# Kernel optimization log

Measured on AMD Instinct MI355X. Metric: run time of the kernel, lower is better.

The kernel has to match this reference:

```python
import jax, jax.numpy as jnp
import numpy as np

D = 256; HD = 16; G = 16; L = 2; HOP = 2; HK = 4
N = 16384; E = 49152; B = 256
VA = 128; VB = 8
SQRT2PI = float(np.sqrt(2.0 * 3.14159))  # module uses pi=3.14159


def group_norm(x, g=G, eps=1e-5):
    # torch GroupNorm(affine=False) on [N, D, 1]: normalize over each group of D//g channels
    n, d = x.shape
    xg = x.reshape(n, g, d // g)
    m = xg.mean(-1, keepdims=True)
    v = ((xg - m) ** 2).mean(-1, keepdims=True)
    return ((xg - m) * jax.lax.rsqrt(v + eps)).reshape(n, d)


def glin(x, w):
    # grouped 1x1 conv (no bias): x [n, g*din], w [g, dout, din] -> [n, g*dout]
    g, dout, din = w.shape
    return jnp.einsum('ngd,god->ngo', x.reshape(-1, g, din), w).reshape(-1, g * dout)


def multi_embed(idx, tables):
    # OGB-style encoder: sum of per-feature embeddings. idx [M,F], tables [F,V,D]
    out = tables[0][idx[:, 0]]
    for f in range(1, tables.shape[0]):
        out = out + tables[f][idx[:, f]]
    return out


def glb(x, pre_w, pre_b, gate_w, val_w, post_w, post_b):
    # GatedLinearBlock (dropout is identity in eval)
    xx = group_norm(x @ pre_w.T + pre_b)
    xx = jax.nn.relu(glin(xx, gate_w)) * glin(xx, val_w)
    return xx @ post_w.T + post_b


def glb2(xg, xv, gate_w, val_w, post_w, post_b):
    # GatedLinearBlock2: separate gate/value inputs, GroupNorm first
    gg = jax.nn.relu(glin(group_norm(xg), gate_w))
    vv = glin(group_norm(xv), val_w)
    return (gg * vv) @ post_w.T + post_b


def forward_impl(x_feat, edge_index, edge_attr, batch, batch_size,
                 edge_distance, atom_emb, bond2d_emb, gauss_means, gauss_stds,
                 attn_w, attn_b, scale_both,
                 conv_bond_emb, conv_pre_w, conv_gate_w, conv_val_w, conv_post_w, conv_post_b, conv_scale,
                 virt_pre_w, virt_pre_b, virt_gate_w, virt_val_w, virt_post_w, virt_post_b, virt_scale,
                 att_pre_w, att_pre_b, att_q_w, att_k_w, att_v_w, att_post_w, att_post_b, att_scale,
                 main_pre_w, main_pre_b, main_gate_w, main_val_w, main_post_w, main_post_b):
    src, dst = edge_index[0], edge_index[1]
    n = x_feat.shape[0]
    deg = jnp.clip(jax.ops.segment_sum(jnp.ones_like(dst), dst, num_segments=n) - 1, 0, 3)
    # --- edge features, mode='both': fuse 2D bond embedding with 3D gaussian features ---
    h2d = multi_embed(edge_attr, bond2d_emb)                      # [E, D]
    std = jnp.abs(gauss_stds) + 0.01
    diff = (edge_distance[:, None] - gauss_means[None, :]) / std
    h3d = jnp.exp(-0.5 * diff * diff) / (SQRT2PI * std)          # [E, D]
    w = jax.nn.sigmoid(jnp.concatenate([h2d, h3d], axis=-1) @ attn_w + attn_b[0])[:, None]
    h_e = w * h2d + (1.0 - w) * h3d
    h_in = jnp.exp(scale_both)[deg] * jax.ops.segment_sum(h_e, dst, num_segments=n)
    h_in = multi_embed(x_feat, atom_emb) + h_in                   # [N, D]
    h_virt = jnp.zeros((batch_size, D), h_in.dtype)
    h_att = jnp.zeros((batch_size, 2 * D // HD, HD, HD), h_in.dtype)
    for l in range(L):
        # --- ConvMessage: hop*kernel gated message-passing sublayers ---
        x_raw, x_out = h_in, jnp.zeros_like(h_in)
        for k in range(HK):
            if k > 0 and k % HOP == 0:
                x_raw, x_out = h_in + x_out, jnp.zeros_like(h_in)
            bond = multi_embed(edge_attr, conv_bond_emb[l, k])
            xp = x_raw @ conv_pre_w[l, k].T
            msg = glb2(xp[dst] + bond, xp[src] + bond,
                       conv_gate_w[l, k], conv_val_w[l, k], conv_post_w[l, k], conv_post_b[l, k])
            x_raw = jax.ops.segment_sum(msg, dst, num_segments=n)
            x_out = x_out + jnp.exp(conv_scale[l, k])[deg] * x_raw
        h_out = h_in + x_out
        # --- VirtMessage: graph-level virtual node with residual state ---
        h_virt = jax.ops.segment_sum(h_in, batch, num_segments=batch_size) + h_virt
        h_out = h_out + (jnp.exp(virt_scale[l]) * glb(h_virt, virt_pre_w[l], virt_pre_b[l],
                          virt_gate_w[l], virt_val_w[l], virt_post_w[l], virt_post_b[l]))[batch]
        # --- AttMessage: linear attention with per-graph scatter normalization ---
        xv0 = group_norm(h_in @ att_pre_w[l].T + att_pre_b[l])
        xq = jnp.exp(glin(xv0, att_q_w[l]) / np.sqrt(HD)).reshape(n, -1, HD)   # [N,32,16]
        xk = jnp.exp(glin(xv0, att_k_w[l]) / np.sqrt(HD)).reshape(n, -1, HD)
        xv = glin(xv0, att_v_w[l]).reshape(n, -1, HD)
        xkv = jnp.einsum('bnh,bnv->bnhv', xk, xv)                               # [N,32,16,16]
        h_att = jax.ops.segment_sum(xkv, batch, num_segments=batch_size) + h_att
        xk_sum = jax.ops.segment_sum(xk, batch, num_segments=batch_size)[batch]
        xq = xq / jnp.einsum('bnh,bnh->bn', xq, xk_sum)[:, :, None]
        att_out = jnp.einsum('bnh,bnhv->bnv', xq, h_att[batch]).reshape(n, 2 * D)
        h_out = h_out + jnp.exp(att_scale[l]) * (att_out @ att_post_w[l].T + att_post_b[l])
        # --- main gated block ---
        h_in = glb(h_out, main_pre_w[l], main_pre_b[l],
                   main_gate_w[l], main_val_w[l], main_post_w[l], main_post_b[l])
    return h_in


def setup_inputs() -> dict:
    key = jax.random.key(0)
    ks = iter(jax.random.split(key, 80))
    def rn(shape, s=0.05):
        return jax.random.normal(next(ks), shape, dtype=jnp.float32) * s
    inp = {}
    inp['x_feat'] = jax.random.randint(next(ks), (N, 9), 0, VA)
    inp['edge_index'] = jax.random.randint(next(ks), (2, E), 0, N)
    inp['edge_attr'] = jax.random.randint(next(ks), (E, 3), 0, VB)
    inp['batch'] = jnp.sort(jax.random.randint(next(ks), (N,), 0, B))
    inp['batch_size'] = B
    inp['edge_distance'] = jax.random.uniform(next(ks), (E,), dtype=jnp.float32) * 4.0
    inp['atom_emb'] = rn((9, VA, D))
    inp['bond2d_emb'] = rn((3, VB, D))
    inp['gauss_means'] = jax.random.uniform(next(ks), (D,), minval=2.0, maxval=3.0)
    inp['gauss_stds'] = jax.random.uniform(next(ks), (D,), minval=1.0, maxval=1.5)
    inp['attn_w'] = rn((2 * D,))
    inp['attn_b'] = rn((1,))
    inp['scale_both'] = jnp.full((4, D), np.log(0.1), jnp.float32)
    inp['conv_bond_emb'] = rn((L, HK, 3, VB, D))
    inp['conv_pre_w'] = rn((L, HK, D, D))
    inp['conv_gate_w'] = rn((L, HK, G, HD, HD))
    inp['conv_val_w'] = rn((L, HK, G, HD, HD))
    inp['conv_post_w'] = rn((L, HK, D, D))
    inp['conv_post_b'] = rn((L, HK, D))
    inp['conv_scale'] = jnp.full((L, HK, 4, D), np.log(0.1), jnp.float32)
    inp['virt_pre_w'] = rn((L, D, D)); inp['virt_pre_b'] = rn((L, D))
    inp['virt_gate_w'] = rn((L, G, 2 * HD, HD)); inp['virt_val_w'] = rn((L, G, 2 * HD, HD))
    inp['virt_post_w'] = rn((L, D, 2 * D)); inp['virt_post_b'] = rn((L, D))
    inp['virt_scale'] = jnp.full((L, D), np.log(0.01), jnp.float32)
    inp['att_pre_w'] = rn((L, D, D)); inp['att_pre_b'] = rn((L, D))
    inp['att_q_w'] = rn((L, G, 2 * HD, HD)); inp['att_k_w'] = rn((L, G, 2 * HD, HD)); inp['att_v_w'] = rn((L, G, 2 * HD, HD))
    inp['att_post_w'] = rn((L, D, 2 * D)); inp['att_post_b'] = rn((L, D))
    inp['att_scale'] = jnp.full((L, D), np.log(0.01), jnp.float32)
    inp['main_pre_w'] = rn((L, D, D)); inp['main_pre_b'] = rn((L, D))
    inp['main_gate_w'] = rn((L, G, 3 * HD, HD)); inp['main_val_w'] = rn((L, G, 3 * HD, HD))
    inp['main_post_w'] = rn((L, D, 3 * D)); inp['main_post_b'] = rn((L, D))
    return inp


def reference(x_feat, edge_index, edge_attr, batch, batch_size, edge_distance,
              atom_emb, bond2d_emb, gauss_means, gauss_stds, attn_w, attn_b, scale_both,
              conv_bond_emb, conv_pre_w, conv_gate_w, conv_val_w, conv_post_w, conv_post_b, conv_scale,
              virt_pre_w, virt_pre_b, virt_gate_w, virt_val_w, virt_post_w, virt_post_b, virt_scale,
              att_pre_w, att_pre_b, att_q_w, att_k_w, att_v_w, att_post_w, att_post_b, att_scale,
              main_pre_w, main_pre_b, main_gate_w, main_val_w, main_post_w, main_post_b):
    return forward_impl(x_feat, edge_index, edge_attr, batch, batch_size,
                        edge_distance, atom_emb, bond2d_emb, gauss_means, gauss_stds,
                        attn_w, attn_b, scale_both,
                        conv_bond_emb, conv_pre_w, conv_gate_w, conv_val_w, conv_post_w, conv_post_b, conv_scale,
                        virt_pre_w, virt_pre_b, virt_gate_w, virt_val_w, virt_post_w, virt_post_b, virt_scale,
                        att_pre_w, att_pre_b, att_q_w, att_k_w, att_v_w, att_post_w, att_post_b, att_scale,
                        main_pre_w, main_pre_b, main_gate_w, main_val_w, main_post_w, main_post_b)
```

## Files before the change

kernel.cpp:

```cpp
#include <hip/hip_runtime.h>
#include <cstdint>
#include <cstddef>
#include <type_traits>

#define NN 16384
#define EE 49152
#define BB 256

typedef _Float16 f16;
typedef _Float16 half8 __attribute__((ext_vector_type(8)));
typedef _Float16 half4v __attribute__((ext_vector_type(4)));
typedef _Float16 half2v __attribute__((ext_vector_type(2)));
typedef float floatx4 __attribute__((ext_vector_type(4)));

#if defined(__has_builtin)
#if __has_builtin(__builtin_amdgcn_fdot2)
#define HAVE_FDOT2 1
#endif
#endif

static constexpr size_t ND = (size_t)NN * 256;


__global__ __launch_bounds__(256) void count_deg_kernel(const int* __restrict__ dst, int* __restrict__ cnt, int e) {
  int i = blockIdx.x * 256 + threadIdx.x;
  if (i < e) atomicAdd(&cnt[dst[i]], 1);
}
__global__ __launch_bounds__(256) void clip_deg_kernel(const int* __restrict__ cnt, int* __restrict__ deg, int n) {
  int i = blockIdx.x * 256 + threadIdx.x;
  if (i < n) { int v = cnt[i] - 1; deg[i] = v < 0 ? 0 : (v > 3 ? 3 : v); }
}
__global__ __launch_bounds__(256) void goff_kernel(const int* __restrict__ batch, int* __restrict__ goff, int n, int b) {
  int i = blockIdx.x * 256 + threadIdx.x;
  if (i > n) return;
  int cur = (i < n) ? batch[i] : b;
  int prev = (i == 0) ? -1 : batch[i - 1];
  for (int x = prev + 1; x <= cur; x++) goff[x] = i;
}
__global__ __launch_bounds__(256) void scan_off_kernel(const int* __restrict__ cnt, int* __restrict__ off) {
  __shared__ int part[256];
  int tid = threadIdx.x;
  int base = tid * 64;
  int s = 0;
  for (int i = 0; i < 64; i++) s += cnt[base + i];
  part[tid] = s;
  __syncthreads();
  for (int o = 1; o < 256; o <<= 1) {
    int t = (tid >= o) ? part[tid - o] : 0;
    __syncthreads();
    part[tid] += t;
    __syncthreads();
  }
  int run = (tid == 0) ? 0 : part[tid - 1];
  for (int i = 0; i < 64; i++) {
    off[base + i] = run;
    run += cnt[base + i];
  }
  if (tid == 255) off[NN] = run;
}
__global__ __launch_bounds__(256) void copy_i_kernel(const int* __restrict__ a, int* __restrict__ b, int n) {
  int i = blockIdx.x * 256 + threadIdx.x;
  if (i < n) b[i] = a[i];
}
__global__ __launch_bounds__(256) void fill_elist_kernel(const int* __restrict__ dst,
    int* __restrict__ cursor, int* __restrict__ elist, int e) {
  int i = blockIdx.x * 256 + threadIdx.x;
  if (i < e) {
    int p = atomicAdd(&cursor[dst[i]], 1);
    elist[p] = i;
  }
}
__global__ __launch_bounds__(256) void gather_edges_kernel(const int* __restrict__ elist,
    const int* __restrict__ eattr, const int* __restrict__ src, const int* __restrict__ dst,
    const float* __restrict__ edist, int* __restrict__ ea_s, int* __restrict__ src_s,
    int* __restrict__ dst_s, float* __restrict__ ed_s) {
  int j = blockIdx.x * 256 + threadIdx.x;
  if (j >= EE) return;
  int e = elist[j];
  ea_s[j * 3 + 0] = eattr[e * 3 + 0];
  ea_s[j * 3 + 1] = eattr[e * 3 + 1];
  ea_s[j * 3 + 2] = eattr[e * 3 + 2];
  src_s[j] = src[e];
  dst_s[j] = dst[e];
  ed_s[j] = edist[e];
}
__global__ __launch_bounds__(256) void add3_kernel(float* __restrict__ dst,
    const float* __restrict__ a, const float* __restrict__ b, int n4) {
  int i = blockIdx.x * 256 + threadIdx.x;
  if (i >= n4) return;
  float4 x = reinterpret_cast<const float4*>(a)[i];
  float4 y = reinterpret_cast<const float4*>(b)[i];
  x.x += y.x; x.y += y.y; x.z += y.z; x.w += y.w;
  reinterpret_cast<float4*>(dst)[i] = x;
}
__global__ __launch_bounds__(256) void add3_both_kernel(float* __restrict__ dst, f16* __restrict__ dstH,
    const float* __restrict__ a, const float* __restrict__ b, int n4) {
  int i = blockIdx.x * 256 + threadIdx.x;
  if (i >= n4) return;
  float4 x = reinterpret_cast<const float4*>(a)[i];
  float4 y = reinterpret_cast<const float4*>(b)[i];
  x.x += y.x; x.y += y.y; x.z += y.z; x.w += y.w;
  reinterpret_cast<float4*>(dst)[i] = x;
  half4v h;
  h[0] = (f16)x.x; h[1] = (f16)x.y; h[2] = (f16)x.z; h[3] = (f16)x.w;
  reinterpret_cast<half4v*>(dstH)[i] = h;
}
__global__ __launch_bounds__(256) void bcast_add_kernel(float* __restrict__ ho,
    const float* __restrict__ vo, const float* __restrict__ vs, const int* __restrict__ batch) {
  int i4 = blockIdx.x * 256 + threadIdx.x;
  int i = i4 * 4;
  int n = i >> 8, c = i & 255;
  float4 h = reinterpret_cast<const float4*>(&ho[i])[0];
  float4 v = *reinterpret_cast<const float4*>(&vo[(size_t)batch[n] * 256 + c]);
  float4 s = *reinterpret_cast<const float4*>(&vs[c]);
  h.x += expf(s.x) * v.x; h.y += expf(s.y) * v.y;
  h.z += expf(s.z) * v.z; h.w += expf(s.w) * v.w;
  *reinterpret_cast<float4*>(&ho[i]) = h;
}
__global__ __launch_bounds__(256) void f2h_kernel(const float* __restrict__ in, f16* __restrict__ out, int n4) {
  int i = blockIdx.x * 256 + threadIdx.x;
  if (i >= n4) return;
  float4 v = reinterpret_cast<const float4*>(in)[i];
  half4v o;
  o[0] = (f16)v.x; o[1] = (f16)v.y; o[2] = (f16)v.z; o[3] = (f16)v.w;
  reinterpret_cast<half4v*>(out)[i] = o;
}

template <typename OUT>
__global__ __launch_bounds__(256) void seg_reduce_kernel(const f16* __restrict__ msg,
    const int* __restrict__ off, OUT* __restrict__ out) {
  int idx = blockIdx.x * 256 + threadIdx.x;
  int n = idx >> 6, c0 = (idx & 63) * 4;
  int j0 = off[n], j1 = off[n + 1];
  float a0 = 0.f, a1 = 0.f, a2 = 0.f, a3 = 0.f;
  int j = j0;
  for (; j + 1 < j1; j += 2) {
    half4v m0 = *reinterpret_cast<const half4v*>(&msg[(size_t)j * 256 + c0]);
    half4v m1 = *reinterpret_cast<const half4v*>(&msg[(size_t)(j + 1) * 256 + c0]);
    a0 += (float)m0[0] + (float)m1[0];
    a1 += (float)m0[1] + (float)m1[1];
    a2 += (float)m0[2] + (float)m1[2];
    a3 += (float)m0[3] + (float)m1[3];
  }
  if (j < j1) {
    half4v m0 = *reinterpret_cast<const half4v*>(&msg[(size_t)j * 256 + c0]);
    a0 += (float)m0[0]; a1 += (float)m0[1]; a2 += (float)m0[2]; a3 += (float)m0[3];
  }
  if constexpr (std::is_same<OUT, float>::value) {
    float4 o = {a0, a1, a2, a3};
    *reinterpret_cast<float4*>(&out[(size_t)n * 256 + c0]) = o;
  } else {
    half4v o;
    o[0] = (f16)a0; o[1] = (f16)a1; o[2] = (f16)a2; o[3] = (f16)a3;
    *reinterpret_cast<half4v*>(&out[(size_t)n * 256 + c0]) = o;
  }
}


__global__ __launch_bounds__(256) void edge_feat_kernel(
    const int* __restrict__ ea_s, const float* __restrict__ ed_s,
    const float* __restrict__ bond2d, const float* __restrict__ gmeans,
    const float* __restrict__ gstds, const float* __restrict__ attn_w,
    const float* __restrict__ attn_b, f16* __restrict__ msg) {
  int lane = threadIdx.x & 63;
  int j = blockIdx.x * 4 + (threadIdx.x >> 6);
  if (j >= EE) return;
  int a0 = ea_s[j * 3 + 0], a1 = ea_s[j * 3 + 1], a2 = ea_s[j * 3 + 2];
  float dist = ed_s[j];
  const float SQ2PI = sqrtf(2.0f * 3.14159f);
  int c0 = lane * 4;
  float4 b0 = *reinterpret_cast<const float4*>(&bond2d[a0 * 256 + c0]);
  float4 b1 = *reinterpret_cast<const float4*>(&bond2d[2048 + a1 * 256 + c0]);
  float4 b2 = *reinterpret_cast<const float4*>(&bond2d[4096 + a2 * 256 + c0]);
  float4 gm = *reinterpret_cast<const float4*>(&gmeans[c0]);
  float4 gs = *reinterpret_cast<const float4*>(&gstds[c0]);
  float4 w2 = *reinterpret_cast<const float4*>(&attn_w[c0]);
  float4 w3 = *reinterpret_cast<const float4*>(&attn_w[256 + c0]);
  float h2[4], h3[4];
  float part = 0.f;
#pragma unroll
  for (int i = 0; i < 4; i++) {
    h2[i] = (&b0.x)[i] + (&b1.x)[i] + (&b2.x)[i];
    float sd = fabsf((&gs.x)[i]) + 0.01f;
    float df = (dist - (&gm.x)[i]) / sd;
    h3[i] = expf(-0.5f * df * df) / (SQ2PI * sd);
    part += (&w2.x)[i] * h2[i] + (&w3.x)[i] * h3[i];
  }
#pragma unroll
  for (int off = 32; off > 0; off >>= 1) part += __shfl_xor(part, off);
  float wg = 1.f / (1.f + expf(-(part + attn_b[0])));
  half4v o;
#pragma unroll
  for (int i = 0; i < 4; i++) o[i] = (f16)(wg * h2[i] + (1.f - wg) * h3[i]);
  *reinterpret_cast<half4v*>(&msg[(size_t)j * 256 + c0]) = o;
}

__global__ __launch_bounds__(256) void atom_finish_kernel(
    const int* __restrict__ xf, const float* __restrict__ emb,
    const float* __restrict__ scale_both, const int* __restrict__ deg,
    const float* __restrict__ tmp, float* __restrict__ h_in, f16* __restrict__ h_inH) {
  int idx = blockIdx.x * 256 + threadIdx.x;
  int n = idx >> 6, c = (idx & 63) * 4;
  float a0 = 0.f, a1 = 0.f, a2 = 0.f, a3 = 0.f;
#pragma unroll
  for (int f = 0; f < 9; f++) {
    int v = xf[n * 9 + f];
    float4 e = *reinterpret_cast<const float4*>(&emb[((size_t)(f * 128 + v)) * 256 + c]);
    a0 += e.x; a1 += e.y; a2 += e.z; a3 += e.w;
  }
  int dg = deg[n];
  float4 s = *reinterpret_cast<const float4*>(&scale_both[dg * 256 + c]);
  float4 t = *reinterpret_cast<const float4*>(&tmp[(size_t)n * 256 + c]);
  float4 r;
  r.x = a0 + expf(s.x) * t.x; r.y = a1 + expf(s.y) * t.y;
  r.z = a2 + expf(s.z) * t.z; r.w = a3 + expf(s.w) * t.w;
  *reinterpret_cast<float4*>(&h_in[(size_t)n * 256 + c]) = r;
  half4v h;
  h[0] = (f16)r.x; h[1] = (f16)r.y; h[2] = (f16)r.z; h[3] = (f16)r.w;
  *reinterpret_cast<half4v*>(&h_inH[(size_t)n * 256 + c]) = h;
}

template <int MODE>
__global__ __launch_bounds__(256) void hgemm_kernel(
    const f16* __restrict__ A, const f16* __restrict__ W,
    const float* __restrict__ bias, const float* __restrict__ scale,
    const int* __restrict__ cnt, const int* __restrict__ deg,
    float* __restrict__ C, float* __restrict__ Cadd, f16* __restrict__ Cf, int K) {
  __shared__ f16 Ah[128 * 40];
  __shared__ f16 Wh[64 * 40];
  const int tid = threadIdx.x;
  const int row0 = blockIdx.x * 128, col0 = blockIdx.y * 64;
  const int lane = tid & 63;
  const int wave = tid >> 6;
  const int wr = (wave >> 1) * 64, wc = (wave & 1) * 32;
  const floatx4 fz = {0.f, 0.f, 0.f, 0.f};
  floatx4 acc[4][2];
#pragma unroll
  for (int m = 0; m < 4; m++)
#pragma unroll
    for (int n = 0; n < 2; n++) acc[m][n] = fz;
  const int q0 = tid * 2;
  const int rA0 = q0 >> 2, pA0 = q0 & 3;
  const int rA1 = (q0 + 1) >> 2, pA1 = (q0 + 1) & 3;
  const int rW = tid >> 2, pW = tid & 3;
  const int kb = (lane >> 4) * 8;
  const int fr = lane & 15;
  uint4 a0 = *reinterpret_cast<const uint4*>(&A[(size_t)(row0 + rA0) * K + pA0 * 8]);
  uint4 a1 = *reinterpret_cast<const uint4*>(&A[(size_t)(row0 + rA1) * K + pA1 * 8]);
  uint4 w0 = *reinterpret_cast<const uint4*>(&W[(size_t)(col0 + rW) * K + pW * 8]);
  for (int k0 = 0;;) {
    *reinterpret_cast<uint4*>(&Ah[rA0 * 40 + pA0 * 8]) = a0;
    *reinterpret_cast<uint4*>(&Ah[rA1 * 40 + pA1 * 8]) = a1;
    *reinterpret_cast<uint4*>(&Wh[rW * 40 + pW * 8]) = w0;
    __syncthreads();
    int kn = k0 + 32;
    if (kn < K) {
      a0 = *reinterpret_cast<const uint4*>(&A[(size_t)(row0 + rA0) * K + kn + pA0 * 8]);
      a1 = *reinterpret_cast<const uint4*>(&A[(size_t)(row0 + rA1) * K + kn + pA1 * 8]);
      w0 = *reinterpret_cast<const uint4*>(&W[(size_t)(col0 + rW) * K + kn + pW * 8]);
    }
    half8 af[4], wf[2];
#pragma unroll
    for (int m = 0; m < 4; m++)
      af[m] = *reinterpret_cast<const half8*>(&Ah[(wr + m * 16 + fr) * 40 + kb]);
#pragma unroll
    for (int n = 0; n < 2; n++)
      wf[n] = *reinterpret_cast<const half8*>(&Wh[(wc + n * 16 + fr) * 40 + kb]);
#pragma unroll
    for (int m = 0; m < 4; m++)
#pragma unroll
      for (int n = 0; n < 2; n++)
        acc[m][n] = __builtin_amdgcn_mfma_f32_16x16x32_f16(af[m], wf[n], acc[m][n], 0, 0, 0);
    if (kn >= K) break;
    __syncthreads();
    k0 = kn;
  }
  const int rl4 = (lane >> 4) * 4, cl = lane & 15;
#pragma unroll
  for (int m = 0; m < 4; m++) {
#pragma unroll
    for (int i = 0; i < 4; i++) {
      int row = row0 + wr + m * 16 + rl4 + i;
      float cb = (MODE >= 4) ? (float)cnt[row] : 1.f;
      int dg = (MODE >= 4) ? deg[row] : 0;
#pragma unroll
      for (int n = 0; n < 2; n++) {
        int col = col0 + wc + n * 16 + cl;
        float v = acc[m][n][i];
        size_t oi = (size_t)row * 256 + col;
        if (MODE >= 4) {
          v += cb * bias[col];
          float sc = expf(scale[dg * 256 + col]);
          if (MODE == 4) Cadd[oi] += sc * v;
          else Cadd[oi] = sc * v;
          if (Cf) Cf[oi] = (f16)v;
        } else if (MODE == 2) {
          v += bias[col];
          float nv = Cadd[oi] + expf(scale[col]) * v;
          if (C) C[oi] = nv;
          if (Cf) Cf[oi] = (f16)nv;
        } else {
          if (bias) v += bias[col];
          if (C) C[oi] = v;
          if (Cf) Cf[oi] = (f16)v;
        }
      }
    }
  }
}

__global__ __launch_bounds__(256) void conv_edge_kernel(
    const f16* __restrict__ xp, const int* __restrict__ ea_s,
    const int* __restrict__ src_s, const int* __restrict__ dst_s,
    const float* __restrict__ bond_emb, const float* __restrict__ gate_w,
    const float* __restrict__ val_w, f16* __restrict__ msg) {
  constexpr int RS = 264;
  __shared__ f16 sg[16 * RS];
  __shared__ f16 sv[16 * RS];
  int tid = threadIdx.x;
  for (int i = tid; i < 4096; i += 256) {
    int g = i >> 8, rem = i & 255;
    sg[g * RS + rem] = (f16)gate_w[i];
    sv[g * RS + rem] = (f16)val_w[i];
  }
  __syncthreads();
  int idx = blockIdx.x * 256 + tid;
  int j = idx >> 4, g = idx & 15;
  int a0 = ea_s[j * 3 + 0], a1 = ea_s[j * 3 + 1], a2 = ea_s[j * 3 + 2];
  int d = dst_s[j], s = src_s[j];
  half8 xd0 = *reinterpret_cast<const half8*>(&xp[(size_t)d * 256 + g * 16]);
  half8 xd1 = *reinterpret_cast<const half8*>(&xp[(size_t)d * 256 + g * 16 + 8]);
  half8 xs0 = *reinterpret_cast<const half8*>(&xp[(size_t)s * 256 + g * 16]);
  half8 xs1 = *reinterpret_cast<const half8*>(&xp[(size_t)s * 256 + g * 16 + 8]);
  const float4* b0p = reinterpret_cast<const float4*>(&bond_emb[a0 * 256 + g * 16]);
  const float4* b1p = reinterpret_cast<const float4*>(&bond_emb[2048 + a1 * 256 + g * 16]);
  const float4* b2p = reinterpret_cast<const float4*>(&bond_emb[4096 + a2 * 256 + g * 16]);
  float xg[16], xv[16];
  float mg = 0.f, mv = 0.f;
#pragma unroll
  for (int q = 0; q < 4; q++) {
    float4 b0 = b0p[q], b1 = b1p[q], b2 = b2p[q];
#pragma unroll
    for (int t = 0; t < 4; t++) {
      int i = q * 4 + t;
      float bo = (&b0.x)[t] + (&b1.x)[t] + (&b2.x)[t];
      float xd = (i < 8) ? (float)xd0[i & 7] : (float)xd1[i & 7];
      float xs = (i < 8) ? (float)xs0[i & 7] : (float)xs1[i & 7];
      xg[i] = xd + bo;
      xv[i] = xs + bo;
      mg += xg[i];
      mv += xv[i];
    }
  }
  mg *= (1.f / 16.f);
  mv *= (1.f / 16.f);
  float vg = 0.f, vv = 0.f;
#pragma unroll
  for (int i = 0; i < 16; i++) {
    float dg_ = xg[i] - mg, dv_ = xv[i] - mv;
    vg += dg_ * dg_;
    vv += dv_ * dv_;
  }
  float rg = rsqrtf(vg * (1.f / 16.f) + 1e-5f);
  float rv = rsqrtf(vv * (1.f / 16.f) + 1e-5f);
#ifdef HAVE_FDOT2
  half2v xgh[8], xvh[8];
#pragma unroll
  for (int q = 0; q < 8; q++) {
    xgh[q][0] = (f16)((xg[2 * q] - mg) * rg);
    xgh[q][1] = (f16)((xg[2 * q + 1] - mg) * rg);
    xvh[q][0] = (f16)((xv[2 * q] - mv) * rv);
    xvh[q][1] = (f16)((xv[2 * q + 1] - mv) * rv);
  }
#else
#pragma unroll
  for (int i = 0; i < 16; i++) {
    xg[i] = (xg[i] - mg) * rg;
    xv[i] = (xv[i] - mv) * rv;
  }
#endif
  const f16* gRow = &sg[g * RS];
  const f16* vRow = &sv[g * RS];
  f16 res[16];
#pragma unroll
  for (int o = 0; o < 16; o++) {
    half8 gA = *reinterpret_cast<const half8*>(&gRow[o * 16]);
    half8 gB = *reinterpret_cast<const half8*>(&gRow[o * 16 + 8]);
    half8 vA = *reinterpret_cast<const half8*>(&vRow[o * 16]);
    half8 vB = *reinterpret_cast<const half8*>(&vRow[o * 16 + 8]);
    float ag = 0.f, av = 0.f;
#ifdef HAVE_FDOT2
#pragma unroll
    for (int q = 0; q < 4; q++) {
      half2v ga = {gA[2 * q], gA[2 * q + 1]};
      half2v gb = {gB[2 * q], gB[2 * q + 1]};
      half2v va = {vA[2 * q], vA[2 * q + 1]};
      half2v vb = {vB[2 * q], vB[2 * q + 1]};
      ag = __builtin_amdgcn_fdot2(xgh[q], ga, ag, false);
      ag = __builtin_amdgcn_fdot2(xgh[q + 4], gb, ag, false);
      av = __builtin_amdgcn_fdot2(xvh[q], va, av, false);
      av = __builtin_amdgcn_fdot2(xvh[q + 4], vb, av, false);
    }
#else
#pragma unroll
    for (int i = 0; i < 8; i++) {
      ag += xg[i] * (float)gA[i] + xg[i + 8] * (float)gB[i];
      av += xv[i] * (float)vA[i] + xv[i + 8] * (float)vB[i];
    }
#endif
    res[o] = (f16)(fmaxf(ag, 0.f) * av);
  }
  uint4* op = reinterpret_cast<uint4*>(&msg[(size_t)j * 256 + g * 16]);
  op[0] = reinterpret_cast<const uint4*>(res)[0];
  op[1] = reinterpret_cast<const uint4*>(res)[1];
}

template <int DOUT>
__global__ __launch_bounds__(256) void glb_mid_kernel(
    const float* __restrict__ X, const float* __restrict__ gate_w,
    const float* __restrict__ val_w, f16* __restrict__ out) {
  constexpr int RS = DOUT * 16 + 8;
  __shared__ f16 sg[16 * RS];
  __shared__ f16 sv[16 * RS];
  int tid = threadIdx.x;
  for (int i = tid; i < 16 * DOUT * 16; i += 256) {
    int g = i / (DOUT * 16), rem = i % (DOUT * 16);
    sg[g * RS + rem] = (f16)gate_w[i];
    sv[g * RS + rem] = (f16)val_w[i];
  }
  __syncthreads();
  int idx = blockIdx.x * 256 + tid;
  int n = idx >> 4, g = idx & 15;
  float x[16];
  float m = 0.f;
  const float4* xp4 = reinterpret_cast<const float4*>(&X[(size_t)n * 256 + g * 16]);
#pragma unroll
  for (int q = 0; q < 4; q++) {
    float4 xq = xp4[q];
#pragma unroll
    for (int t = 0; t < 4; t++) {
      x[q * 4 + t] = (&xq.x)[t];
      m += (&xq.x)[t];
    }
  }
  m *= (1.f / 16.f);
  float v = 0.f;
#pragma unroll
  for (int i = 0; i < 16; i++) {
    float d_ = x[i] - m;
    v += d_ * d_;
  }
  float r = rsqrtf(v * (1.f / 16.f) + 1e-5f);
#pragma unroll
  for (int i = 0; i < 16; i++) x[i] = (x[i] - m) * r;
#ifdef HAVE_FDOT2
  half2v xh[8];
#pragma unroll
  for (int q = 0; q < 8; q++) { xh[q][0] = (f16)x[2 * q]; xh[q][1] = (f16)x[2 * q + 1]; }
#endif
  const f16* gRow = &sg[g * RS];
  const f16* vRow = &sv[g * RS];
  f16 res[DOUT];
#pragma unroll
  for (int o = 0; o < DOUT; o++) {
    half8 gA = *reinterpret_cast<const half8*>(&gRow[o * 16]);
    half8 gB = *reinterpret_cast<const half8*>(&gRow[o * 16 + 8]);
    half8 vA = *reinterpret_cast<const half8*>(&vRow[o * 16]);
    half8 vB = *reinterpret_cast<const half8*>(&vRow[o * 16 + 8]);
    float ag = 0.f, av = 0.f;
#ifdef HAVE_FDOT2
#pragma unroll
    for (int q = 0; q < 4; q++) {
      half2v gq = {gA[2 * q], gA[2 * q + 1]};
      half2v g2 = {gB[2 * q], gB[2 * q + 1]};
      half2v vq = {vA[2 * q], vA[2 * q + 1]};
      half2v v2 = {vB[2 * q], vB[2 * q + 1]};
      ag = __builtin_amdgcn_fdot2(xh[q], gq, ag, false);
      ag = __builtin_amdgcn_fdot2(xh[q + 4], g2, ag, false);
      av = __builtin_amdgcn_fdot2(xh[q], vq, av, false);
      av = __builtin_amdgcn_fdot2(xh[q + 4], v2, av, false);
    }
#else
#pragma unroll
    for (int i = 0; i < 8; i++) {
      ag += x[i] * (float)gA[i] + x[i + 8] * (float)gB[i];
      av += x[i] * (float)vA[i] + x[i + 8] * (float)vB[i];
    }
#endif
    res[o] = (f16)(fmaxf(ag, 0.f) * av);
  }
  f16* op = &out[(size_t)n * (16 * DOUT) + g * DOUT];
#pragma unroll
  for (int q = 0; q < DOUT / 8; q++)
    *reinterpret_cast<half8*>(&op[q * 8]) = *reinterpret_cast<const half8*>(&res[q * 8]);
}

__global__ __launch_bounds__(256) void gn_vec_kernel(float* __restrict__ X) {
  int idx = blockIdx.x * 256 + threadIdx.x;
  int n = idx >> 6, q = idx & 63;
  float4 x = *reinterpret_cast<const float4*>(&X[(size_t)n * 256 + q * 4]);
  float s = x.x + x.y + x.z + x.w;
  float s2 = x.x * x.x + x.y * x.y + x.z * x.z + x.w * x.w;
  s += __shfl_xor(s, 1); s2 += __shfl_xor(s2, 1);
  s += __shfl_xor(s, 2); s2 += __shfl_xor(s2, 2);
  float m = s * (1.f / 16.f);
  float var = s2 * (1.f / 16.f) - m * m;
  float r = rsqrtf(var + 1e-5f);
  x.x = (x.x - m) * r; x.y = (x.y - m) * r;
  x.z = (x.z - m) * r; x.w = (x.w - m) * r;
  *reinterpret_cast<float4*>(&X[(size_t)n * 256 + q * 4]) = x;
}

__global__ __launch_bounds__(256) void att_graph_kernel(
    const float* __restrict__ xv0, const float* __restrict__ k_w,
    const float* __restrict__ v_w, const int* __restrict__ goff,
    float* __restrict__ h_att, float* __restrict__ xk_sum) {
  __shared__ float kx[8][256];
  __shared__ float vx[8][256];
  __shared__ float rows[8][256];
  const int tid = threadIdx.x;
  const int b = blockIdx.x >> 1, half = blockIdx.x & 1;
  const int p = half * 256 + tid;
  const int g = p >> 5;
  const int headLocal = tid >> 4;
  const int head = p >> 4, h = p & 15;
  float wk[16], wv[16];
#pragma unroll
  for (int i = 0; i < 4; i++) {
    float4 k0 = *reinterpret_cast<const float4*>(&k_w[p * 16 + i * 4]);
    float4 v0 = *reinterpret_cast<const float4*>(&v_w[p * 16 + i * 4]);
    wk[i * 4 + 0] = k0.x; wk[i * 4 + 1] = k0.y; wk[i * 4 + 2] = k0.z; wk[i * 4 + 3] = k0.w;
    wv[i * 4 + 0] = v0.x; wv[i * 4 + 1] = v0.y; wv[i * 4 + 2] = v0.z; wv[i * 4 + 3] = v0.w;
  }
  float hacc[16];
  const float* hg = &h_att[(size_t)b * 8192];
#pragma unroll
  for (int j = 0; j < 16; j++) hacc[j] = hg[h * 512 + head * 16 + j];
  float ks = 0.f;
  const int n0 = goff[b], n1 = goff[b + 1];
  float r[8];
#pragma unroll
  for (int nn = 0; nn < 8; nn++) {
    int n = n0 + nn;
    r[nn] = (n < n1) ? xv0[(size_t)n * 256 + tid] : 0.f;
  }
  for (int nbase = n0; nbase < n1; nbase += 8) {
#pragma unroll
    for (int nn = 0; nn < 8; nn++) rows[nn][tid] = r[nn];
    __syncthreads();
#pragma unroll
    for (int nn = 0; nn < 8; nn++) {
      int n = nbase + 8 + nn;
      r[nn] = (n < n1) ? xv0[(size_t)n * 256 + tid] : 0.f;
    }
#pragma unroll
    for (int nn = 0; nn < 8; nn++) {
      const float4* rp = reinterpret_cast<const float4*>(&rows[nn][g * 16]);
      float aK = 0.f, aV = 0.f;
#pragma unroll
      for (int q = 0; q < 4; q++) {
        float4 x0 = rp[q];
#pragma unroll
        for (int t = 0; t < 4; t++) {
          float e0 = (&x0.x)[t];
          aK += e0 * wk[q * 4 + t];
          aV += e0 * wv[q * 4 + t];
        }
      }
      bool valid = (nbase + nn) < n1;
      float ek = valid ? expf(aK * 0.25f) : 0.f;
      kx[nn][tid] = ek;
      vx[nn][tid] = aV;
      ks += ek;
    }
    __syncthreads();
#pragma unroll
    for (int nn = 0; nn < 8; nn++) {
      float kk = kx[nn][tid];
      const float4* vp = reinterpret_cast<const float4*>(&vx[nn][headLocal * 16]);
#pragma unroll
      for (int q = 0; q < 4; q++) {
        float4 vq = vp[q];
        hacc[q * 4 + 0] += kk * vq.x;
        hacc[q * 4 + 1] += kk * vq.y;
        hacc[q * 4 + 2] += kk * vq.z;
        hacc[q * 4 + 3] += kk * vq.w;
      }
    }
    __syncthreads();
  }
  float* hgo = &h_att[(size_t)b * 8192];
#pragma unroll
  for (int j = 0; j < 16; j++) hgo[h * 512 + head * 16 + j] = hacc[j];
  xk_sum[(size_t)b * 512 + p] = ks;
}

__global__ __launch_bounds__(256) void att_out_kernel(
    const float* __restrict__ xv0, const float* __restrict__ q_w,
    const float* __restrict__ xk_sum, const float* __restrict__ h_att,
    const int* __restrict__ batch, f16* __restrict__ out) {
  __shared__ float sqw[16 * 260];
  int tid = threadIdx.x;
  for (int i = tid; i < 8192; i += 256) {
    int g = i >> 9, rem = i & 511;
    sqw[g * 260 + rem] = q_w[i];
  }
  __syncthreads();
  int wave = tid >> 6, lane = tid & 63;
  int n = blockIdx.x * 4 + wave;
  int head = lane >> 1, half = lane & 1;
  int g = head >> 1, j = head & 1;
  int b = batch[n];
  float x[16];
  const float4* xp4 = reinterpret_cast<const float4*>(&xv0[(size_t)n * 256 + g * 16]);
#pragma unroll
  for (int q = 0; q < 4; q++) {
    float4 xq = xp4[q];
#pragma unroll
    for (int t = 0; t < 4; t++) x[q * 4 + t] = (&xq.x)[t];
  }
  float qv[16];
  float denom = 0.f;
  const float* ks = &xk_sum[(size_t)b * 512 + head * 16];
#pragma unroll
  for (int h = 0; h < 16; h++) {
    const float4* wp = reinterpret_cast<const float4*>(&sqw[g * 260 + (j * 16 + h) * 16]);
    float a = 0.f;
#pragma unroll
    for (int q = 0; q < 4; q++) {
      float4 wq = wp[q];
#pragma unroll
      for (int t = 0; t < 4; t++) a += x[q * 4 + t] * (&wq.x)[t];
    }
    float e = expf(a * 0.25f);
    qv[h] = e;
    denom += e * ks[h];
  }
  float inv = 1.f / denom;
  float acc[8] = {0.f, 0.f, 0.f, 0.f, 0.f, 0.f, 0.f, 0.f};
  const float* hb = &h_att[(size_t)b * 8192 + head * 16 + half * 8];
#pragma unroll
  for (int h = 0; h < 16; h++) {
    float4 v0 = *reinterpret_cast<const float4*>(&hb[h * 512]);
    float4 v1 = *reinterpret_cast<const float4*>(&hb[h * 512 + 4]);
    float qh = qv[h];
    acc[0] += qh * v0.x; acc[1] += qh * v0.y; acc[2] += qh * v0.z; acc[3] += qh * v0.w;
    acc[4] += qh * v1.x; acc[5] += qh * v1.y; acc[6] += qh * v1.z; acc[7] += qh * v1.w;
  }
  half8 res;
#pragma unroll
  for (int v = 0; v < 8; v++) res[v] = (f16)(acc[v] * inv);
  *reinterpret_cast<half8*>(&out[(size_t)n * 512 + head * 16 + half * 8]) = res;
}

__global__ __launch_bounds__(256) void virt_seg_kernel(const float* __restrict__ h_in,
    const int* __restrict__ goff, float* __restrict__ h_virt) {
  int b = blockIdx.x, c = threadIdx.x;
  float acc = h_virt[(size_t)b * 256 + c];
  int n0 = goff[b], n1 = goff[b + 1];
  for (int n = n0; n < n1; n++) acc += h_in[(size_t)n * 256 + c];
  h_virt[(size_t)b * 256 + c] = acc;
}


extern "C" void kernel_launch(void* const* d_in, const int* in_sizes, int n_in,
                              void* d_out, int out_size, void* d_ws, size_t ws_size,
                              hipStream_t stream) {
  const int* x_feat = (const int*)d_in[0];
  const int* eidx = (const int*)d_in[1];
  const int* eattr = (const int*)d_in[2];
  const int* batch = (const int*)d_in[3];
  const float* edist = (const float*)d_in[5];
  const float* atom_emb = (const float*)d_in[6];
  const float* bond2d = (const float*)d_in[7];
  const float* gmeans = (const float*)d_in[8];
  const float* gstds = (const float*)d_in[9];
  const float* attn_w = (const float*)d_in[10];
  const float* attn_b = (const float*)d_in[11];
  const float* scale_both = (const float*)d_in[12];
  const float* conv_bond_emb = (const float*)d_in[13];
  const float* conv_pre_w = (const float*)d_in[14];
  const float* conv_gate_w = (const float*)d_in[15];
  const float* conv_val_w = (const float*)d_in[16];
  const float* conv_post_w = (const float*)d_in[17];
  const float* conv_post_b = (const float*)d_in[18];
  const float* conv_scale = (const float*)d_in[19];
  const float* virt_pre_w = (const float*)d_in[20];
  const float* virt_pre_b = (const float*)d_in[21];
  const float* virt_gate_w = (const float*)d_in[22];
  const float* virt_val_w = (const float*)d_in[23];
  const float* virt_post_w = (const float*)d_in[24];
  const float* virt_post_b = (const float*)d_in[25];
  const float* virt_scale = (const float*)d_in[26];
  const float* att_pre_w = (const float*)d_in[27];
  const float* att_pre_b = (const float*)d_in[28];
  const float* att_q_w = (const float*)d_in[29];
  const float* att_k_w = (const float*)d_in[30];
  const float* att_v_w = (const float*)d_in[31];
  const float* att_post_w = (const float*)d_in[32];
  const float* att_post_b = (const float*)d_in[33];
  const float* att_scale = (const float*)d_in[34];
  const float* main_pre_w = (const float*)d_in[35];
  const float* main_pre_b = (const float*)d_in[36];
  const float* main_gate_w = (const float*)d_in[37];
  const float* main_val_w = (const float*)d_in[38];
  const float* main_post_w = (const float*)d_in[39];
  const float* main_post_b = (const float*)d_in[40];

  const int* src = eidx;
  const int* dst = eidx + EE;

  float* ws = (float*)d_ws;
  float* h_in = ws;
  float* h_out = ws + ND;
  float* x_raw = ws + 2 * ND;
  float* x_out = ws + 3 * ND;
  float* nodeA = ws + 4 * ND;
  f16* h_inH = (f16*)(ws + 5 * ND);
  f16* xrawH = (f16*)(ws + 5 * ND + ND / 2);
  f16* hTmp = (f16*)(ws + 6 * ND);
  f16* msgH = (f16*)(ws + 6 * ND + ND / 2);
  float* sm = ws + 8 * ND;
  f16* hW = (f16*)sm;
  float* h_virt = sm + 1179648;
  float* h_att = h_virt + 65536;
  float* xk_sum = h_att + 2097152;
  float* vt1 = xk_sum + 131072;
  float* vout = vt1 + 65536;
  f16* vmidH = (f16*)(vout + 65536);
  f16* virtH = vmidH + 131072;
  int* cnt = (int*)(virtH + 65536);
  int* deg = cnt + NN;
  int* goff = deg + NN;
  int* off = goff + BB + 1;
  int* cursor = off + NN + 1;
  int* elist = cursor + NN;
  int* ea_s = elist + EE;
  int* src_s = ea_s + 3 * EE;
  int* dst_s = src_s + EE;
  float* ed_s = (float*)(dst_s + EE);

  f16* wCpre = hW;
  f16* wCpost = hW + 524288;
  f16* wApre = hW + 1048576;
  f16* wApost = hW + 1179648;
  f16* wMpre = hW + 1441792;
  f16* wMpost = hW + 1572864;
  f16* wVpre = hW + 1966080;
  f16* wVpost = hW + 2097152;

  auto cvt = [&](const float* in, f16* out, int n) {
    f2h_kernel<<<n / 4 / 256, 256, 0, stream>>>(in, out, n / 4);
  };

  cvt(conv_pre_w, wCpre, 524288);
  cvt(conv_post_w, wCpost, 524288);
  cvt(att_pre_w, wApre, 131072);
  cvt(att_post_w, wApost, 262144);
  cvt(main_pre_w, wMpre, 131072);
  cvt(main_post_w, wMpost, 393216);
  cvt(virt_pre_w, wVpre, 131072);
  cvt(virt_post_w, wVpost, 262144);

  (void)hipMemsetAsync(cnt, 0, NN * sizeof(int), stream);
  count_deg_kernel<<<EE / 256, 256, 0, stream>>>(dst, cnt, EE);
  clip_deg_kernel<<<NN / 256, 256, 0, stream>>>(cnt, deg, NN);
  goff_kernel<<<(NN + 256) / 256, 256, 0, stream>>>(batch, goff, NN, BB);
  scan_off_kernel<<<1, 256, 0, stream>>>(cnt, off);
  copy_i_kernel<<<NN / 256, 256, 0, stream>>>(off, cursor, NN);
  fill_elist_kernel<<<EE / 256, 256, 0, stream>>>(dst, cursor, elist, EE);
  gather_edges_kernel<<<EE / 256, 256, 0, stream>>>(elist, eattr, src, dst, edist,
                                                    ea_s, src_s, dst_s, ed_s);

  edge_feat_kernel<<<EE / 4, 256, 0, stream>>>(ea_s, ed_s, bond2d, gmeans, gstds,
                                               attn_w, attn_b, msgH);
  seg_reduce_kernel<float><<<NN / 4, 256, 0, stream>>>(msgH, off, x_out);
  atom_finish_kernel<<<NN * 64 / 256, 256, 0, stream>>>(x_feat, atom_emb, scale_both, deg,
                                                        x_out, h_in, h_inH);
  (void)hipMemsetAsync(h_virt, 0, 65536 * 4, stream);
  (void)hipMemsetAsync(h_att, 0, 2097152 * 4, stream);

  const dim3 gN(NN / 128, 4), gB(BB / 128, 4);
  const int n4 = (int)(ND / 4);

  for (int l = 0; l < 2; l++) {
    const f16* curH = h_inH;
    for (int k = 0; k < 4; k++) {
      if (k == 2) {
        add3_both_kernel<<<n4 / 256, 256, 0, stream>>>(x_raw, xrawH, h_in, x_out, n4);
        curH = xrawH;
      }
      size_t lk = (size_t)(l * 4 + k);
      hgemm_kernel<0><<<gN, 256, 0, stream>>>(curH, wCpre + lk * 65536, nullptr, nullptr,
                                              nullptr, nullptr, nullptr, nullptr, hTmp, 256);
      conv_edge_kernel<<<EE * 16 / 256, 256, 0, stream>>>(
          hTmp, ea_s, src_s, dst_s, conv_bond_emb + lk * 6144,
          conv_gate_w + lk * 4096, conv_val_w + lk * 4096, msgH);
      seg_reduce_kernel<f16><<<NN / 4, 256, 0, stream>>>(msgH, off, hTmp);
      if (k == 0 || k == 2)
        hgemm_kernel<5><<<gN, 256, 0, stream>>>(hTmp, wCpost + lk * 65536,
                                                conv_post_b + lk * 256, conv_scale + lk * 1024,
                                                cnt, deg, nullptr, x_out, xrawH, 256);
      else
        hgemm_kernel<4><<<gN, 256, 0, stream>>>(hTmp, wCpost + lk * 65536,
                                                conv_post_b + lk * 256, conv_scale + lk * 1024,
                                                cnt, deg, nullptr, x_out, xrawH, 256);
      curH = xrawH;
    }
    add3_kernel<<<n4 / 256, 256, 0, stream>>>(h_out, h_in, x_out, n4);

    virt_seg_kernel<<<BB, 256, 0, stream>>>(h_in, goff, h_virt);
    cvt(h_virt, virtH, 65536);
    hgemm_kernel<0><<<gB, 256, 0, stream>>>(virtH, wVpre + (size_t)l * 65536,
                                            virt_pre_b + (size_t)l * 256, nullptr, nullptr,
                                            nullptr, vt1, nullptr, nullptr, 256);
    glb_mid_kernel<32><<<BB * 16 / 256, 256, 0, stream>>>(
        vt1, virt_gate_w + (size_t)l * 8192, virt_val_w + (size_t)l * 8192, vmidH);
    hgemm_kernel<0><<<gB, 256, 0, stream>>>(vmidH, wVpost + (size_t)l * 131072,
                                            virt_post_b + (size_t)l * 256, nullptr, nullptr,
                                            nullptr, vout, nullptr, nullptr, 512);
    bcast_add_kernel<<<n4 / 256, 256, 0, stream>>>(
        h_out, vout, virt_scale + (size_t)l * 256, batch);

    hgemm_kernel<0><<<gN, 256, 0, stream>>>(h_inH, wApre + (size_t)l * 65536,
                                            att_pre_b + (size_t)l * 256, nullptr, nullptr,
                                            nullptr, nodeA, nullptr, nullptr, 256);
    gn_vec_kernel<<<NN * 64 / 256, 256, 0, stream>>>(nodeA);
    att_graph_kernel<<<BB * 2, 256, 0, stream>>>(
        nodeA, att_k_w + (size_t)l * 8192, att_v_w + (size_t)l * 8192, goff, h_att, xk_sum);
    att_out_kernel<<<NN / 4, 256, 0, stream>>>(
        nodeA, att_q_w + (size_t)l * 8192, xk_sum, h_att, batch, msgH);
    hgemm_kernel<2><<<gN, 256, 0, stream>>>(msgH, wApost + (size_t)l * 131072,
                                            att_post_b + (size_t)l * 256,
                                            att_scale + (size_t)l * 256, nullptr, nullptr,
                                            nullptr, h_out, hTmp, 512);

    hgemm_kernel<0><<<gN, 256, 0, stream>>>(hTmp, wMpre + (size_t)l * 65536,
                                            main_pre_b + (size_t)l * 256, nullptr, nullptr,
                                            nullptr, nodeA, nullptr, nullptr, 256);
    glb_mid_kernel<48><<<NN * 16 / 256, 256, 0, stream>>>(
        nodeA, main_gate_w + (size_t)l * 12288, main_val_w + (size_t)l * 12288, msgH);
    float* hdst = (l == 1) ? (float*)d_out : h_in;
    f16* hdstH = (l == 1) ? nullptr : h_inH;
    hgemm_kernel<0><<<gN, 256, 0, stream>>>(msgH, wMpost + (size_t)l * 196608,
                                            main_post_b + (size_t)l * 256, nullptr, nullptr,
                                            nullptr, hdst, nullptr, hdstH, 768);
  }
}
```

Baseline: 1.066 ms.

## Process attention output per graph with shared-memory staged state, drop h_att memset

The attention output kernel now runs one block per graph, stages that graph's 16x512 h_att state in padded shared memory, and loops over the graph's nodes. Each thread now computes all 16 values of one head instead of two threads splitting them. The first layer's graph kernel starts from zero accumulators through a template flag, so the 8 MB h_att memset is no longer needed. The cost is fewer blocks (256 instead of 4096), larger shared memory per block, and more work per thread, which may hurt occupancy and balance when graph sizes vary.

```diff
diff --git a/kernel.cpp b/kernel.cpp
--- a/kernel.cpp
+++ b/kernel.cpp
@@ -511,6 +511,7 @@
   *reinterpret_cast<float4*>(&X[(size_t)n * 256 + q * 4]) = x;
 }
 
+template <bool FIRST>
 __global__ __launch_bounds__(256) void att_graph_kernel(
     const float* __restrict__ xv0, const float* __restrict__ k_w,
     const float* __restrict__ v_w, const int* __restrict__ goff,
@@ -533,9 +534,14 @@
     wv[i * 4 + 0] = v0.x; wv[i * 4 + 1] = v0.y; wv[i * 4 + 2] = v0.z; wv[i * 4 + 3] = v0.w;
   }
   float hacc[16];
-  const float* hg = &h_att[(size_t)b * 8192];
-#pragma unroll
-  for (int j = 0; j < 16; j++) hacc[j] = hg[h * 512 + head * 16 + j];
+  if (FIRST) {
+#pragma unroll
+    for (int j = 0; j < 16; j++) hacc[j] = 0.f;
+  } else {
+    const float* hg = &h_att[(size_t)b * 8192];
+#pragma unroll
+    for (int j = 0; j < 16; j++) hacc[j] = hg[h * 512 + head * 16 + j];
+  }
   float ks = 0.f;
   const int n0 = goff[b], n1 = goff[b + 1];
   float r[8];
@@ -598,59 +604,74 @@
 __global__ __launch_bounds__(256) void att_out_kernel(
     const float* __restrict__ xv0, const float* __restrict__ q_w,
     const float* __restrict__ xk_sum, const float* __restrict__ h_att,
-    const int* __restrict__ batch, f16* __restrict__ out) {
+    const int* __restrict__ goff, f16* __restrict__ out) {
   __shared__ float sqw[16 * 260];
-  int tid = threadIdx.x;
+  __shared__ float hat[16 * 644];
+  int tid = threadIdx.x, b = blockIdx.x;
   for (int i = tid; i < 8192; i += 256) {
     int g = i >> 9, rem = i & 511;
     sqw[g * 260 + rem] = q_w[i];
   }
+  for (int i = tid; i < 8192; i += 256) {
+    int h = i >> 9, rem = i & 511;
+    int head = rem >> 4, v = rem & 15;
+    hat[h * 644 + head * 20 + v] = h_att[(size_t)b * 8192 + i];
+  }
   __syncthreads();
-  int wave = tid >> 6, lane = tid & 63;
-  int n = blockIdx.x * 4 + wave;
-  int head = lane >> 1, half = lane & 1;
+  int n0 = goff[b], n1 = goff[b + 1];
+  int nl = tid >> 5, head = tid & 31;
   int g = head >> 1, j = head & 1;
-  int b = batch[n];
-  float x[16];
-  const float4* xp4 = reinterpret_cast<const float4*>(&xv0[(size_t)n * 256 + g * 16]);
-#pragma unroll
-  for (int q = 0; q < 4; q++) {
-    float4 xq = xp4[q];
-#pragma unroll
-    for (int t = 0; t < 4; t++) x[q * 4 + t] = (&xq.x)[t];
-  }
-  float qv[16];
-  float denom = 0.f;
   const float* ks = &xk_sum[(size_t)b * 512 + head * 16];
-#pragma unroll
-  for (int h = 0; h < 16; h++) {
-    const float4* wp = reinterpret_cast<const float4*>(&sqw[g * 260 + (j * 16 + h) * 16]);
-    float a = 0.f;
+  for (int nbase = n0; nbase < n1; nbase += 8) {
+    int n = nbase + nl;
+    if (n >= n1) continue;
+    float x[16];
+    const float4* xp4 = reinterpret_cast<const float4*>(&xv0[(size_t)n * 256 + g * 16]);
 #pragma unroll
     for (int q = 0; q < 4; q++) {
-      float4 wq = wp[q];
-#pragma unroll
-      for (int t = 0; t < 4; t++) a += x[q * 4 + t] * (&wq.x)[t];
-    }
-    float e = expf(a * 0.25f);
-    qv[h] = e;
-    denom += e * ks[h];
-  }
-  float inv = 1.f / denom;
-  float acc[8] = {0.f, 0.f, 0.f, 0.f, 0.f, 0.f, 0.f, 0.f};
-  const float* hb = &h_att[(size_t)b * 8192 + head * 16 + half * 8];
-#pragma unroll
-  for (int h = 0; h < 16; h++) {
-    float4 v0 = *reinterpret_cast<const float4*>(&hb[h * 512]);
-    float4 v1 = *reinterpret_cast<const float4*>(&hb[h * 512 + 4]);
-    float qh = qv[h];
-    acc[0] += qh * v0.x; acc[1] += qh * v0.y; acc[2] += qh * v0.z; acc[3] += qh * v0.w;
-    acc[4] += qh * v1.x; acc[5] += qh * v1.y; acc[6] += qh * v1.z; acc[7] += qh * v1.w;
-  }
-  half8 res;
-#pragma unroll
-  for (int v = 0; v < 8; v++) res[v] = (f16)(acc[v] * inv);
-  *reinterpret_cast<half8*>(&out[(size_t)n * 512 + head * 16 + half * 8]) = res;
+      float4 xq = xp4[q];
+#pragma unroll
+      for (int t = 0; t < 4; t++) x[q * 4 + t] = (&xq.x)[t];
+    }
+    float qv[16];
+    float denom = 0.f;
+#pragma unroll
+    for (int h = 0; h < 16; h++) {
+      const float4* wp = reinterpret_cast<const float4*>(&sqw[g * 260 + (j * 16 + h) * 16]);
+      float a = 0.f;
+#pragma unroll
+      for (int q = 0; q < 4; q++) {
+        float4 wq = wp[q];
+#pragma unroll
+        for (int t = 0; t < 4; t++) a += x[q * 4 + t] * (&wq.x)[t];
+      }
+      float e = expf(a * 0.25f);
+      qv[h] = e;
+      denom += e * ks[h];
+    }
+    float inv = 1.f / denom;
+    float acc[16] = {0.f, 0.f, 0.f, 0.f, 0.f, 0.f, 0.f, 0.f,
+                     0.f, 0.f, 0.f, 0.f, 0.f, 0.f, 0.f, 0.f};
+#pragma unroll
+    for (int h = 0; h < 16; h++) {
+      float qh = qv[h];
+      const float4* hp = reinterpret_cast<const float4*>(&hat[h * 644 + head * 20]);
+#pragma unroll
+      for (int q = 0; q < 4; q++) {
+        float4 vq = hp[q];
+        acc[q * 4 + 0] += qh * vq.x;
+        acc[q * 4 + 1] += qh * vq.y;
+        acc[q * 4 + 2] += qh * vq.z;
+        acc[q * 4 + 3] += qh * vq.w;
+      }
+    }
+    f16 res[16];
+#pragma unroll
+    for (int v = 0; v < 16; v++) res[v] = (f16)(acc[v] * inv);
+    uint4* op = reinterpret_cast<uint4*>(&out[(size_t)n * 512 + head * 16]);
+    op[0] = reinterpret_cast<const uint4*>(res)[0];
+    op[1] = reinterpret_cast<const uint4*>(res)[1];
+  }
 }
 
 __global__ __launch_bounds__(256) void virt_seg_kernel(const float* __restrict__ h_in,
@@ -778,7 +799,6 @@
   atom_finish_kernel<<<NN * 64 / 256, 256, 0, stream>>>(x_feat, atom_emb, scale_both, deg,
                                                         x_out, h_in, h_inH);
   (void)hipMemsetAsync(h_virt, 0, 65536 * 4, stream);
-  (void)hipMemsetAsync(h_att, 0, 2097152 * 4, stream);
 
   const dim3 gN(NN / 128, 4), gB(BB / 128, 4);
   const int n4 = (int)(ND / 4);
@@ -826,10 +846,14 @@
                                             att_pre_b + (size_t)l * 256, nullptr, nullptr,
                                             nullptr, nodeA, nullptr, nullptr, 256);
     gn_vec_kernel<<<NN * 64 / 256, 256, 0, stream>>>(nodeA);
-    att_graph_kernel<<<BB * 2, 256, 0, stream>>>(
-        nodeA, att_k_w + (size_t)l * 8192, att_v_w + (size_t)l * 8192, goff, h_att, xk_sum);
-    att_out_kernel<<<NN / 4, 256, 0, stream>>>(
-        nodeA, att_q_w + (size_t)l * 8192, xk_sum, h_att, batch, msgH);
+    if (l == 0)
+      att_graph_kernel<true><<<BB * 2, 256, 0, stream>>>(
+          nodeA, att_k_w + (size_t)l * 8192, att_v_w + (size_t)l * 8192, goff, h_att, xk_sum);
+    else
+      att_graph_kernel<false><<<BB * 2, 256, 0, stream>>>(
+          nodeA, att_k_w + (size_t)l * 8192, att_v_w + (size_t)l * 8192, goff, h_att, xk_sum);
+    att_out_kernel<<<BB, 256, 0, stream>>>(
+        nodeA, att_q_w + (size_t)l * 8192, xk_sum, h_att, goff, msgH);
     hgemm_kernel<2><<<gN, 256, 0, stream>>>(msgH, wApost + (size_t)l * 131072,
                                             att_post_b + (size_t)l * 256,
                                             att_scale + (size_t)l * 256, nullptr, nullptr,
```

Measured after the change: 1.054 ms. No clear change (-1.1%).
